# Optimization experiments

Hardware: AMD Instinct MI355X
Metric: run time of the kernel (lower is better)

## Reference

```python
import jax, jax.numpy as jnp
import numpy as np

FP8_MAX = 448.0  # e4m3 max
SCALE_MARGIN = 0.8


def _fp8_quant_dequant(t, scale):
    # scaled value is <= 448*0.8 by construction, so no saturation/overflow
    q = (t / scale).astype(jnp.float8_e4m3fn)
    return q.astype(jnp.float32) * scale


def setup_inputs() -> dict:
    key = jax.random.key(0)
    k1, k2 = jax.random.split(key)
    B, S, D_IN, D_OUT = 4, 2048, 2048, 2048
    x = jax.random.normal(k1, (B, S, D_IN), dtype=jnp.float32)
    weight = jax.random.normal(k2, (D_OUT, D_IN), dtype=jnp.float32)
    bias = jnp.zeros((D_OUT,), dtype=jnp.float32)
    return {"x": x, "weight": weight, "bias": bias}


def reference(x, weight, bias):
    # Shared FP8ScalingManager: amax history = [amax_x] for x, then [amax_x, amax_w] for w.
    amax_x = jnp.max(jnp.abs(x))
    amax_w = jnp.max(jnp.abs(weight))
    x_scale = amax_x / (FP8_MAX * SCALE_MARGIN)
    w_scale = jnp.maximum(amax_x, amax_w) / (FP8_MAX * SCALE_MARGIN)  # history max
    x_scale = jax.lax.stop_gradient(x_scale)  # .item() detaches in torch
    w_scale = jax.lax.stop_gradient(w_scale)
    # quantize to fp8 e4m3, dequantize, scaled matmul (math of torch._scaled_mm)
    x_dq = _fp8_quant_dequant(x, x_scale)      # [B,S,Din]
    w_dq = _fp8_quant_dequant(weight, w_scale)  # [Dout,Din]
    out = jnp.einsum('bsd,od->bso', x_dq, w_dq)  # [B,S,Dout]
    return out + bias
```

## Files before the change

kernel.cpp:

```cpp
#include <hip/hip_runtime.h>
#include <stdint.h>

typedef float v4f __attribute__((ext_vector_type(4)));
typedef int v8i __attribute__((ext_vector_type(8)));

#define FP8_DENOM 358.4f


__device__ __forceinline__ unsigned pack4_fp8(float a, float b, float c, float d) {
  int v = 0;
  v = __builtin_amdgcn_cvt_pk_fp8_f32(a, b, v, false);
  v = __builtin_amdgcn_cvt_pk_fp8_f32(c, d, v, true);
  return (unsigned)v;
}

__device__ __forceinline__ void gload_lds16(const void* g, void* l) {
  __builtin_amdgcn_global_load_lds(
      (const __attribute__((address_space(1))) uint32_t*)(uintptr_t)g,
      (__attribute__((address_space(3))) uint32_t*)(uint32_t)(uintptr_t)l,
      16, 0, 0);
}


__global__ void amax2_kernel(const float4* __restrict__ x, int nx4,
                             const float4* __restrict__ w, int nw4,
                             int xblocks, unsigned* __restrict__ out) {
  const int isw = ((int)blockIdx.x >= xblocks) ? 1 : 0;
  const float4* p = isw ? w : x;
  const int n4 = isw ? nw4 : nx4;
  const int b0 = isw ? ((int)blockIdx.x - xblocks) : (int)blockIdx.x;
  const int nb = isw ? ((int)gridDim.x - xblocks) : xblocks;
  float m = 0.f;
  const long stride = (long)nb * blockDim.x;
  for (long i = (long)b0 * blockDim.x + threadIdx.x; i < n4; i += stride) {
    float4 v = p[i];
    m = fmaxf(m, fmaxf(fmaxf(fabsf(v.x), fabsf(v.y)), fmaxf(fabsf(v.z), fabsf(v.w))));
  }
#pragma unroll
  for (int off = 32; off > 0; off >>= 1)
    m = fmaxf(m, __shfl_down(m, off, 64));
  __shared__ float red[4];
  const int lane = threadIdx.x & 63, wvid = threadIdx.x >> 6;
  if (lane == 0) red[wvid] = m;
  __syncthreads();
  if (threadIdx.x == 0) {
    float mm = fmaxf(fmaxf(red[0], red[1]), fmaxf(red[2], red[3]));
    atomicMax(out + isw, __float_as_uint(mm));
  }
}


__global__ void quant2_kernel(const float4* __restrict__ x, uint4* __restrict__ xq, int nx16,
                              const float4* __restrict__ w, uint4* __restrict__ wq, int nw16,
                              int xblocks, const unsigned* __restrict__ amax) {
  const float ax = __uint_as_float(amax[0]);
  const float aw = __uint_as_float(amax[1]);
  const int isw = ((int)blockIdx.x >= xblocks) ? 1 : 0;
  const float scale = isw ? (fmaxf(ax, aw) / FP8_DENOM) : (ax / FP8_DENOM);
  const float4* in = isw ? w : x;
  uint4* outq = isw ? wq : xq;
  const int n16 = isw ? nw16 : nx16;
  const int b0 = isw ? ((int)blockIdx.x - xblocks) : (int)blockIdx.x;
  const int nb = isw ? ((int)gridDim.x - xblocks) : xblocks;
  const long stride = (long)nb * blockDim.x;
  for (long i = (long)b0 * blockDim.x + threadIdx.x; i < n16; i += stride) {
    float4 v0 = in[4 * i + 0], v1 = in[4 * i + 1], v2 = in[4 * i + 2], v3 = in[4 * i + 3];
    uint4 r;
    r.x = pack4_fp8(v0.x / scale, v0.y / scale, v0.z / scale, v0.w / scale);
    r.y = pack4_fp8(v1.x / scale, v1.y / scale, v1.z / scale, v1.w / scale);
    r.z = pack4_fp8(v2.x / scale, v2.y / scale, v2.z / scale, v2.w / scale);
    r.w = pack4_fp8(v3.x / scale, v3.y / scale, v3.z / scale, v3.w / scale);
    outq[i] = r;
  }
}


__global__ void __launch_bounds__(256) gemm_mx(
    const uint8_t* __restrict__ Aq, const uint8_t* __restrict__ Bq,
    const float* __restrict__ bias, float* __restrict__ out,
    const unsigned* __restrict__ amax) {
  constexpr int K = 2048, N = 2048, BK = 128;
  __shared__ alignas(16) uint8_t sA[128 * BK];
  __shared__ alignas(16) uint8_t sB[128 * BK];

  const int tid = threadIdx.x;
  const int lane = tid & 63;
  const int wid = tid >> 6;
  const int wy = wid >> 1, wx = wid & 1;
  const long tileM = (long)blockIdx.y * 128;
  const long tileN = (long)blockIdx.x * 128;

  v4f acc[4][4];
#pragma unroll
  for (int i = 0; i < 4; ++i)
#pragma unroll
    for (int j = 0; j < 4; ++j) acc[i][j] = (v4f)(0.f);

  const int srow = tid >> 3;
  const int schunk = (tid & 7) ^ (srow & 7);
  const uint8_t* gA = Aq + (tileM + srow) * K + schunk * 16;
  const uint8_t* gB = Bq + (tileN + srow) * K + schunk * 16;

  const int q = lane >> 4;
  const int mrow = lane & 15;

  int aoff[4][2], boff[4][2];
#pragma unroll
  for (int i = 0; i < 4; ++i) {
    const int rA = wy * 64 + i * 16 + mrow, swA = rA & 7;
    aoff[i][0] = rA * 128 + 16 * ((2 * q) ^ swA);
    aoff[i][1] = rA * 128 + 16 * ((2 * q + 1) ^ swA);
    const int rB = wx * 64 + i * 16 + mrow, swB = rB & 7;
    boff[i][0] = rB * 128 + 16 * ((2 * q) ^ swB);
    boff[i][1] = rB * 128 + 16 * ((2 * q + 1) ^ swB);
  }

  for (int k0 = 0; k0 < K; k0 += BK) {
#pragma unroll
    for (int s = 0; s < 4; ++s) {
      gload_lds16(gA + (long)s * 32 * K + k0, sA + s * 4096 + tid * 16);
      gload_lds16(gB + (long)s * 32 * K + k0, sB + s * 4096 + tid * 16);
    }
    __syncthreads();

    union Frag { v8i v; uint4 h[2]; };
    Frag a[4], b[4];
#pragma unroll
    for (int i = 0; i < 4; ++i) {
      a[i].h[0] = *(const uint4*)(sA + aoff[i][0]);
      a[i].h[1] = *(const uint4*)(sA + aoff[i][1]);
      b[i].h[0] = *(const uint4*)(sB + boff[i][0]);
      b[i].h[1] = *(const uint4*)(sB + boff[i][1]);
    }
#pragma unroll
    for (int i = 0; i < 4; ++i)
#pragma unroll
      for (int j = 0; j < 4; ++j)
        acc[i][j] = __builtin_amdgcn_mfma_scale_f32_16x16x128_f8f6f4(
            a[i].v, b[j].v, acc[i][j],  0,  0,
             0, 0x7F7F7F7F,  0, 0x7F7F7F7F);
    __syncthreads();
  }

  const float ax = __uint_as_float(amax[0]);
  const float aw = __uint_as_float(amax[1]);
  const float scale = (ax / FP8_DENOM) * (fmaxf(ax, aw) / FP8_DENOM);
#pragma unroll
  for (int j = 0; j < 4; ++j) {
    const long col = tileN + wx * 64 + j * 16 + mrow;
    const float bv = bias[col];
#pragma unroll
    for (int i = 0; i < 4; ++i) {
      const long row = tileM + wy * 64 + i * 16 + q * 4;
#pragma unroll
      for (int r = 0; r < 4; ++r)
        out[(row + r) * N + col] = acc[i][j][r] * scale + bv;
    }
  }
}


extern "C" void kernel_launch(void* const* d_in, const int* in_sizes, int n_in,
                              void* d_out, int out_size, void* d_ws, size_t ws_size,
                              hipStream_t stream) {
  const float* x = (const float*)d_in[0];
  const float* w = (const float*)d_in[1];
  const float* bias = (const float*)d_in[2];
  float* out = (float*)d_out;

  const int M = 8192, N = 2048, K = 2048;
  const long nx = (long)M * K, nw = (long)N * K;

  unsigned* amax = (unsigned*)d_ws;
  uint8_t* xq = (uint8_t*)d_ws + 256;
  uint8_t* wq = xq + nx;

  hipMemsetAsync(d_ws, 0, 8, stream);

  amax2_kernel<<<4096, 256, 0, stream>>>((const float4*)x, (int)(nx / 4),
                                         (const float4*)w, (int)(nw / 4), 3072, amax);
  quant2_kernel<<<5120, 256, 0, stream>>>((const float4*)x, (uint4*)xq, (int)(nx / 16),
                                          (const float4*)w, (uint4*)wq, (int)(nw / 16),
                                          4096, amax);
  gemm_mx<<<dim3(N / 128, M / 128), 256, 0, stream>>>(xq, wq, bias, out, amax);
}
```

Measured before the change: 213.7 us.

## Replace atomic amax with two-stage partial reduction and drop memset

The amax pass now writes one per-block partial maximum, with each block covering a fixed 4096-float4 chunk through unrolled independent loads. A single-block kernel then reduces the partials into the x and w amax values. This removes the hipMemsetAsync call and the global atomics, and gives more memory-level parallelism per thread. The cost is an extra tiny kernel launch, and the chunk sizes are hardcoded to these exact shapes.

```diff
diff --git a/kernel.cpp b/kernel.cpp
--- a/kernel.cpp
+++ b/kernel.cpp
@@ -22,30 +22,53 @@
 }
 
 
-__global__ void amax2_kernel(const float4* __restrict__ x, int nx4,
-                             const float4* __restrict__ w, int nw4,
-                             int xblocks, unsigned* __restrict__ out) {
-  const int isw = ((int)blockIdx.x >= xblocks) ? 1 : 0;
-  const float4* p = isw ? w : x;
-  const int n4 = isw ? nw4 : nx4;
-  const int b0 = isw ? ((int)blockIdx.x - xblocks) : (int)blockIdx.x;
-  const int nb = isw ? ((int)gridDim.x - xblocks) : xblocks;
-  float m = 0.f;
-  const long stride = (long)nb * blockDim.x;
-  for (long i = (long)b0 * blockDim.x + threadIdx.x; i < n4; i += stride) {
-    float4 v = p[i];
-    m = fmaxf(m, fmaxf(fmaxf(fabsf(v.x), fabsf(v.y)), fmaxf(fabsf(v.z), fabsf(v.w))));
-  }
+__global__ void __launch_bounds__(256) amax_part(const float4* __restrict__ x,
+                                                 const float4* __restrict__ w,
+                                                 float* __restrict__ part) {
+  const int b = blockIdx.x, t = threadIdx.x;
+  const float4* p = (b < 1024) ? x : w;
+  const long base = (long)((b < 1024) ? b : (b - 1024)) * 4096;
+  float m0 = 0.f, m1 = 0.f, m2 = 0.f, m3 = 0.f;
+#pragma unroll
+  for (int j = 0; j < 4; ++j) {
+    float4 v0 = p[base + (j * 4 + 0) * 256 + t];
+    float4 v1 = p[base + (j * 4 + 1) * 256 + t];
+    float4 v2 = p[base + (j * 4 + 2) * 256 + t];
+    float4 v3 = p[base + (j * 4 + 3) * 256 + t];
+    m0 = fmaxf(m0, fmaxf(fmaxf(fabsf(v0.x), fabsf(v0.y)), fmaxf(fabsf(v0.z), fabsf(v0.w))));
+    m1 = fmaxf(m1, fmaxf(fmaxf(fabsf(v1.x), fabsf(v1.y)), fmaxf(fabsf(v1.z), fabsf(v1.w))));
+    m2 = fmaxf(m2, fmaxf(fmaxf(fabsf(v2.x), fabsf(v2.y)), fmaxf(fabsf(v2.z), fabsf(v2.w))));
+    m3 = fmaxf(m3, fmaxf(fmaxf(fabsf(v3.x), fabsf(v3.y)), fmaxf(fabsf(v3.z), fabsf(v3.w))));
+  }
+  float m = fmaxf(fmaxf(m0, m1), fmaxf(m2, m3));
 #pragma unroll
   for (int off = 32; off > 0; off >>= 1)
     m = fmaxf(m, __shfl_down(m, off, 64));
   __shared__ float red[4];
-  const int lane = threadIdx.x & 63, wvid = threadIdx.x >> 6;
+  const int lane = t & 63, wvid = t >> 6;
   if (lane == 0) red[wvid] = m;
   __syncthreads();
-  if (threadIdx.x == 0) {
-    float mm = fmaxf(fmaxf(red[0], red[1]), fmaxf(red[2], red[3]));
-    atomicMax(out + isw, __float_as_uint(mm));
+  if (t == 0) part[b] = fmaxf(fmaxf(red[0], red[1]), fmaxf(red[2], red[3]));
+}
+
+
+__global__ void __launch_bounds__(256) scale_reduce(const float* __restrict__ part,
+                                                    unsigned* __restrict__ amax) {
+  const int t = threadIdx.x;
+  float mx = fmaxf(fmaxf(part[t], part[t + 256]), fmaxf(part[t + 512], part[t + 768]));
+  float mw = part[1024 + t];
+#pragma unroll
+  for (int off = 32; off > 0; off >>= 1) {
+    mx = fmaxf(mx, __shfl_down(mx, off, 64));
+    mw = fmaxf(mw, __shfl_down(mw, off, 64));
+  }
+  __shared__ float rx[4], rw[4];
+  const int lane = t & 63, wvid = t >> 6;
+  if (lane == 0) { rx[wvid] = mx; rw[wvid] = mw; }
+  __syncthreads();
+  if (t == 0) {
+    amax[0] = __float_as_uint(fmaxf(fmaxf(rx[0], rx[1]), fmaxf(rx[2], rx[3])));
+    amax[1] = __float_as_uint(fmaxf(fmaxf(rw[0], rw[1]), fmaxf(rw[2], rw[3])));
   }
 }
 
@@ -172,13 +195,12 @@
   const long nx = (long)M * K, nw = (long)N * K;
 
   unsigned* amax = (unsigned*)d_ws;
-  uint8_t* xq = (uint8_t*)d_ws + 256;
+  float* part = (float*)((uint8_t*)d_ws + 256);
+  uint8_t* xq = (uint8_t*)d_ws + 8192;
   uint8_t* wq = xq + nx;
 
-  hipMemsetAsync(d_ws, 0, 8, stream);
-
-  amax2_kernel<<<4096, 256, 0, stream>>>((const float4*)x, (int)(nx / 4),
-                                         (const float4*)w, (int)(nw / 4), 3072, amax);
+  amax_part<<<1280, 256, 0, stream>>>((const float4*)x, (const float4*)w, part);
+  scale_reduce<<<1, 256, 0, stream>>>(part, amax);
   quant2_kernel<<<5120, 256, 0, stream>>>((const float4*)x, (uint4*)xq, (int)(nx / 16),
                                           (const float4*)w, (uint4*)wq, (int)(nw / 16),
                                           4096, amax);
```

Measured after the change: 179.6 us. -15.9%, faster.
